# Performance work log

Hardware: AMD Instinct MI355X
Metric: run time of the kernel (lower is better)

Reference implementation:

```python
import jax, jax.numpy as jnp
import numpy as np

B, N, D = 8, 500, 256
H, W = 480, 640
NUM_CORNERS = 500
MATCH_RADIUS = 1.0
SCORE_RADIUS = 8
BETA = (1.0, 1.0, 1.0)


def _rodrigues(aa):
    theta = jnp.linalg.norm(aa, axis=-1, keepdims=True)
    k = aa / jnp.maximum(theta, 1e-8)
    kx, ky, kz = k[..., 0], k[..., 1], k[..., 2]
    z = jnp.zeros_like(kx)
    Km = jnp.stack([jnp.stack([z, -kz, ky], -1),
                    jnp.stack([kz, z, -kx], -1),
                    jnp.stack([-ky, kx, z], -1)], -2)
    th = theta[..., None]
    return jnp.eye(3) + jnp.sin(th) * Km + (1. - jnp.cos(th)) * (Km @ Km)


def setup_inputs() -> dict:
    key = jax.random.key(0)
    ks = jax.random.split(key, 8)
    descriptors = jax.random.normal(ks[0], (B, N, D), jnp.float32)
    points = jax.random.uniform(ks[1], (B, N, 2), jnp.float32, -1.0, 1.0)
    pointness = jax.random.uniform(ks[2], (B, 1, H, W), jnp.float32) * 0.98 + 0.01
    depths_dense = jax.random.uniform(ks[3], (B, 1, H, W), jnp.float32) * 4.0 + 1.0
    imgs = jax.random.uniform(ks[4], (B, 3, H, W), jnp.float32)
    aa = jax.random.normal(ks[5], (B, 3), jnp.float32) * 0.02
    t = jax.random.normal(ks[6], (B, 3), jnp.float32) * 0.05
    R = _rodrigues(aa)
    poses = jnp.tile(jnp.eye(4, dtype=jnp.float32), (B, 1, 1))
    poses = poses.at[:, :3, :3].set(R).at[:, :3, 3].set(t)
    Kmat = jnp.tile(jnp.array([[300., 0., W / 2.], [0., 300., H / 2.], [0., 0., 1.]], jnp.float32), (B, 1, 1))
    return {"descriptors": descriptors, "points": points, "pointness": pointness,
            "depths_dense": depths_dense, "poses": poses, "K": Kmat, "imgs": imgs}


def denormalize(pts, h, w):
    return jnp.stack([(pts[..., 0] + 1.) * 0.5 * (w - 1), (pts[..., 1] + 1.) * 0.5 * (h - 1)], -1)


def normalize_pix(pts, h, w):
    return jnp.stack([2. * pts[..., 0] / (w - 1) - 1., 2. * pts[..., 1] / (h - 1) - 1.], -1)


def bilinear_sample(img, px):  # img (H,W), px (...,2) pixel coords
    x = jnp.clip(px[..., 0], 0., W - 1.)
    y = jnp.clip(px[..., 1], 0., H - 1.)
    x0 = jnp.floor(x); y0 = jnp.floor(y)
    x1 = jnp.minimum(x0 + 1., W - 1.); y1 = jnp.minimum(y0 + 1., H - 1.)
    wx = x - x0; wy = y - y0
    x0i = x0.astype(jnp.int32); x1i = x1.astype(jnp.int32)
    y0i = y0.astype(jnp.int32); y1i = y1.astype(jnp.int32)
    v00 = img[y0i, x0i]; v01 = img[y0i, x1i]
    v10 = img[y1i, x0i]; v11 = img[y1i, x1i]
    return v00 * (1 - wx) * (1 - wy) + v01 * wx * (1 - wy) + v10 * (1 - wx) * wy + v11 * wx * wy


def pairwise_project(pts, depths, poses, Kmat):
    # pts (B,N,2) normalized; proj[i,j] = points of frame i projected into frame j
    px = denormalize(pts, H, W)
    d = jax.vmap(bilinear_sample)(depths[:, 0], px)  # (B,Np)
    Kinv = jnp.linalg.inv(Kmat)
    homog = jnp.concatenate([px, jnp.ones_like(px[..., :1])], -1)
    Xc = d[..., None] * jnp.einsum('bij,bnj->bni', Kinv, homog)
    Rm = poses[:, :3, :3]; t = poses[:, :3, 3]
    Xw = jnp.einsum('bij,bnj->bni', Rm, Xc) + t[:, None, :]
    diff = Xw[:, None, :, :] - t[None, :, None, :]           # (src,dst,Np,3)
    Xj = jnp.einsum('jba,ijnb->ijna', Rm, diff)              # R_j^T (Xw - t_j)
    uvw = jnp.einsum('jab,ijnb->ijna', Kmat, Xj)
    z = uvw[..., 2]
    zs = jnp.where(jnp.abs(z) < 1e-6, 1e-6, z)
    pn = normalize_pix(jnp.stack([uvw[..., 0] / zs, uvw[..., 1] / zs], -1), H, W)
    invis = (z <= 1e-6) | (jnp.abs(pn[..., 0]) > 1.) | (jnp.abs(pn[..., 1]) > 1.) | (d[:, None, :] <= 0.)
    return pn, invis


def conv2d_same(x, k):
    return jax.lax.conv_general_dilated(x, k[None, None].astype(x.dtype), (1, 1), 'SAME')


_SOBEL_X = np.array([[-1, 0, 1], [-2, 0, 2], [-1, 0, 1]], np.float32) / 8.


def _gauss_kernel(size=7, sigma=1.0):
    r = np.arange(size) - size // 2
    g = np.exp(-r ** 2 / (2 * sigma ** 2)); g /= g.sum()
    return np.outer(g, g).astype(np.float32)


_GAUSS = _gauss_kernel()


def gftt_response(gray):  # min-eigenvalue (Shi-Tomasi) corner response
    gx = conv2d_same(gray, jnp.asarray(_SOBEL_X))
    gy = conv2d_same(gray, jnp.asarray(_SOBEL_X.T))
    g = jnp.asarray(_GAUSS)
    dx2 = conv2d_same(gx * gx, g)
    dy2 = conv2d_same(gy * gy, g)
    dxy = conv2d_same(gx * gy, g)
    tr = dx2 + dy2
    det = dx2 * dy2 - dxy * dxy
    return 0.5 * (tr - jnp.sqrt(jnp.clip(tr * tr - 4. * det, 0.)))


def nms2d(x, k=5):
    mp = jax.lax.reduce_window(x, -jnp.inf, jax.lax.max, (1, 1, k, k), (1, 1, 1, 1), 'SAME')
    return x * (x == mp).astype(x.dtype)


def get_corners(imgs, depths, poses, Kmat):
    gray = (0.299 * imgs[:, 0] + 0.587 * imgs[:, 1] + 0.114 * imgs[:, 2])[:, None]
    c = nms2d(gftt_response(gray))
    r = SCORE_RADIUS
    blocks = c.reshape(B, 1, H // r, r, W // r, r)  # unfold/fold with stride==kernel
    bm = blocks.max(axis=(3, 5), keepdims=True)
    blocks = blocks * ((blocks > 0) & (blocks == bm)).astype(c.dtype)
    c = blocks.reshape(B, 1, H, W)
    vals, idx = jax.lax.top_k(c.reshape(B, -1), NUM_CORNERS)
    xs = (idx % W).astype(jnp.float32)
    ys = (idx // W).astype(jnp.float32)
    coords = normalize_pix(jnp.stack([xs, ys], -1), H, W)
    proj, invis = pairwise_project(coords, depths, poses, Kmat)
    proj = jnp.where(invis[..., None], -2.0, proj)
    combined = jnp.transpose(proj, (1, 0, 2, 3)).reshape(B, B * NUM_CORNERS, 2)  # per dst frame
    pix = jnp.round(denormalize(combined, H, W)).astype(jnp.int32)
    wq, hq = pix[..., 0], pix[..., 1]
    valid = wq >= 0
    v = jnp.tile(vals.reshape(-1), B).reshape(B, B * NUM_CORNERS)
    v = jnp.where(valid, v, 0.)
    hc = jnp.clip(hq, 0, H - 1)
    wc = jnp.clip(wq, 0, W - 1)
    bidx = jnp.broadcast_to(jnp.arange(B)[:, None], (B, B * NUM_CORNERS))
    target = jnp.zeros((B, H, W), imgs.dtype).at[bidx, hc, wc].max(v)
    target = nms2d(target[:, None])
    return (target > 0).astype(imgs.dtype)


def distinction_loss(desc):
    dn = desc / jnp.clip(jnp.linalg.norm(desc, axis=-1, keepdims=True), 1e-8)
    c = jnp.einsum('bnd,bmd->bnm', dn, dn)
    return jax.nn.relu(c).mean()


def match_loss(desc, points, proj, invis):
    p_src = denormalize(jax.lax.stop_gradient(points), H, W)  # (B,N,2)
    p_dst = denormalize(jax.lax.stop_gradient(proj), H, W)    # (src a, dst b, N, 2)
    diff = p_src[None, :, :, None, :] - p_dst[:, :, None, :, :]  # (a,b,n,m,2)
    m = (diff ** 2).sum(-1) <= MATCH_RADIUS ** 2
    m = m & (~invis)[:, :, :, None]                 # zero invisible rows
    n_idx = jnp.arange(N)
    m = m & (n_idx[:, None] < n_idx[None, :])       # triu(diagonal=1)
    dn = desc / jnp.clip(jnp.linalg.norm(desc, axis=-1, keepdims=True), 1e-8)
    cos = jnp.einsum('bnd,amd->abnm', dn, dn)       # cosine(desc[b,n], desc[a,m])
    mf = m.astype(desc.dtype)
    cnt = jnp.maximum(mf.sum(), 1.)
    return ((1. - cos) * mf).sum() / cnt


def bce(p, t):
    logp = jnp.maximum(jnp.log(p), -100.)
    log1p = jnp.maximum(jnp.log(1. - p), -100.)
    return -(t * logp + (1. - t) * log1p).mean()


def reference(descriptors, points, pointness, depths_dense, poses, K, imgs):
    distinction = distinction_loss(descriptors)
    target = get_corners(imgs, depths_dense, poses, K)
    cornerness = bce(pointness, target)
    proj, invis = pairwise_project(points, depths_dense, poses, K)
    match = match_loss(descriptors, points, proj, invis)
    return BETA[0] * distinction + BETA[1] * cornerness + BETA[2] * match
```

## Files before the change

kernel.cpp:

```cpp
#include <hip/hip_runtime.h>
#include <math.h>

#define BB 8
#define NN 500
#define DDIM 256
#define HH 480
#define WW 640
#define HWSZ (HH*WW)
#define BHW (BB*HWSZ)
#define NBLK 4800
#define NOVF 3392
#define NLIST (BB*NN*BB)
#define NBCE2 512
#define NCORR 125
#define NDM 66

#define PD_DIST  0
#define PD_MS    512
#define PD_MC    1024
#define PD_BCE   1536
#define PD_CORR  2560
#define PD_TOTAL 2688

typedef __attribute__((ext_vector_type(8))) short short8;
typedef __attribute__((ext_vector_type(4))) float f32x4;


static __device__ __forceinline__ float wredmaxf(float v) {
  #pragma unroll
  for (int o = 1; o < 64; o <<= 1) v = fmaxf(v, __shfl_xor(v, o, 64));
  return v;
}

static __device__ __forceinline__ double blockRedSum256(double v) {
  __shared__ double sp[4];
  __syncthreads();
  #pragma unroll
  for (int o = 32; o > 0; o >>= 1) v += __shfl_down(v, o, 64);
  int lane = threadIdx.x & 63, wid = threadIdx.x >> 6;
  if (lane == 0) sp[wid] = v;
  __syncthreads();
  double r = 0.0;
  if (threadIdx.x == 0) r = sp[0] + sp[1] + sp[2] + sp[3];
  return r;
}

static __device__ __forceinline__ unsigned short f2bf(float f) {
  unsigned u = __float_as_uint(f);
  return (unsigned short)((u + 0x7FFFu + ((u >> 16) & 1u)) >> 16);
}

static __device__ __forceinline__ float bilin(const float* __restrict__ img, float px, float py) {
  float x = fminf(fmaxf(px, 0.0f), 639.0f);
// ... 61 lines not shown
                                               float* __restrict__ psrc, float* __restrict__ pdst,
                                               int* __restrict__ minv,
                                               const float* __restrict__ pn, double* __restrict__ pd) {
  __shared__ float smem[6536];
  __shared__ float Gw[7];
  int bid = blockIdx.x, tid = threadIdx.x;
  if (bid < 2400) {
    float* sgxy = smem;
    float* gray = smem + 2888;
    float* hxx  = smem + 2888;
    float* hyy  = hxx + 1216;
    float* hxy  = hyy + 1216;
    int b = bid / 300, r = bid % 300;
    int byi = r / 20, bxi = r % 20;
    int bx = bxi*32, by = byi*32;
    if (bid < 20) {
      int g = bid*256 + tid;
      if (g == 0) *done = 0;
      for (int e = g; e < BB*64; e += 20*256) ovf[e] = 0;
      for (int e = g; e < NLIST; e += 20*256) list[e] = -1;
      for (int e = g; e < 12288; e += 20*256) {
        int bi = e / 1536, rr2 = e % 1536;
        dnb_u[(bi*512 + 500)*128 + rr2] = 0u;
      }
    }
    if (tid < 7) {
      double g[7]; double s = 0.0;
      for (int q = 0; q < 7; q++) { double rr2 = (double)(q-3); g[q] = exp(-(rr2*rr2)/2.0); s += g[q]; }
      Gw[tid] = (float)(g[tid]/s);
    }
    const float* ib = imgs + (size_t)b*3*HWSZ;
    for (int e = tid; e < 40*40; e += 256) {
      int ly = e/40, lx = e%40;
      int X = bx - 4 + lx, Y = by - 4 + ly;
      float v = 0.f;
      if (X>=0 && X<WW && Y>=0 && Y<HH) {
        int p = Y*WW + X;
        v = 0.299f*ib[p] + 0.587f*ib[HWSZ+p] + 0.114f*ib[2*HWSZ+p];
      }
      gray[ly*41+lx] = v;
    }
    __syncthreads();
    const float kxw[3][3] = {{-0.125f,0.f,0.125f},{-0.25f,0.f,0.25f},{-0.125f,0.f,0.125f}};
    for (int e = tid; e < 38*38; e += 256) {
      int rr2 = e/38, c = e%38;
      int X = bx - 3 + c, Y = by - 3 + rr2;
      float sx = 0.f, sy = 0.f;
      #pragma unroll
      for (int i = 0; i < 3; i++)
        #pragma unroll
        for (int j = 0; j < 3; j++) {
          float v = gray[(rr2+i)*41 + (c+j)];
          sx += kxw[i][j]*v;
          sy += kxw[j][i]*v;
        }
      bool in = (X>=0 && X<WW && Y>=0 && Y<HH);
      sgxy[e*2]   = in ? sx : 0.f;
      sgxy[e*2+1] = in ? sy : 0.f;
    }
    __syncthreads();
    for (int e = tid; e < 38*32; e += 256) {
      int rr2 = e >> 5, co = e & 31;
      int base = (rr2*38 + co)*2;
      float axx = 0.f, ayy = 0.f, axy = 0.f;
      #pragma unroll
      for (int j = 0; j < 7; j++) {
        float a = sgxy[base + j*2];
        float c = sgxy[base + j*2 + 1];
        float Gj = Gw[j];
        axx += Gj*(a*a); ayy += Gj*(c*c); axy += Gj*(a*c);
      }
      hxx[e] = axx; hyy[e] = ayy; hxy[e] = axy;
    }
    __syncthreads();
    int tx = tid & 31, ty = tid >> 5;
    int r0 = ty*4;
    float axx[4] = {0,0,0,0}, ayy[4] = {0,0,0,0}, axy[4] = {0,0,0,0};
    #pragma unroll
    for (int rr2 = 0; rr2 < 10; rr2++) {
      int rr3 = r0 + rr2;
      float vxx = hxx[rr3*32+tx], vyy = hyy[rr3*32+tx], vxy = hxy[rr3*32+tx];
      #pragma unroll
      for (int o = 0; o < 4; o++) {
        int i = rr2 - o;
        if (i >= 0 && i <= 6) {
          float Gi = Gw[i];
          axx[o] += Gi*vxx; ayy[o] += Gi*vyy; axy[o] += Gi*vxy;
        }
      }
    }
    #pragma unroll
    for (int o = 0; o < 4; o++) {
      float tr = axx[o] + ayy[o];
      float det = axx[o]*ayy[o] - axy[o]*axy[o];
      float disc = fmaxf(tr*tr - 4.0f*det, 0.f);
      int y = by + r0 + o;
      resp[(size_t)b*HWSZ + y*WW + (bx+tx)] = 0.5f*(tr - sqrtf(disc));
    }
  } else if (bid < 6400) {
    int row = bid - 2400;
    float v = desc[(size_t)row*DDIM + tid];
    float* sp2 = smem;
    float s = v*v;
    #pragma unroll
    for (int o = 32; o > 0; o >>= 1) s += __shfl_down(s, o, 64);
    int lane = tid & 63, wid = tid >> 6;
    if (lane == 0) sp2[wid] = s;
    __syncthreads();
    if (tid == 0) sp2[4] = fmaxf(sqrtf(sp2[0]+sp2[1]+sp2[2]+sp2[3]), 1e-8f);
    __syncthreads();
    float o = v / sp2[4];
    dn[(size_t)row*DDIM + tid] = o;
    int pr = (row/500)*512 + (row%500);
    dnb[(size_t)pr*DDIM + tid] = f2bf(o);
  } else if (bid < 6416) {
    int t = (bid - 6400)*256 + tid;
    if (t < BB*NN) {
      int a = t / NN, m = t % NN;
      float p0 = points[t*2], p1 = points[t*2+1];
      float px = (p0 + 1.0f)*0.5f*639.0f;
      float py = (p1 + 1.0f)*0.5f*479.0f;
      float Xw[3], d;
      src_compute(px, py, depths + (size_t)a*HWSZ, poses, Km, a, Xw, &d);
      psrc[t*2] = px; psrc[t*2+1] = py;
      for (int b = 0; b < BB; b++) {
        float nx, ny; bool inv;
        project_to(poses, Km, b, Xw, d, &nx, &ny, &inv);
        int o = (a*BB + b)*NN + m;
        pdst[o*2]   = (nx + 1.0f)*0.5f*639.0f;
        pdst[o*2+1] = (ny + 1.0f)*0.5f*479.0f;
        minv[o] = inv ? 1 : 0;
      }
    }
  } else {
    int blk = bid - 6416;
    int g = blk*256 + tid;
    double l = 0.0;
    for (int q = g; q < BHW/4; q += NBCE2*256) {
      float4 v = ((const float4*)pn)[q];
      l -= (double)fmaxf(logf(1.f - v.x), -100.f);
      l -= (double)fmaxf(logf(1.f - v.y), -100.f);
      l -= (double)fmaxf(logf(1.f - v.z), -100.f);
      l -= (double)fmaxf(logf(1.f - v.w), -100.f);
    }
    double s = blockRedSum256(l);
    if (tid == 0) pd[PD_BCE + blk] = s;
  }
}

__global__ __launch_bounds__(256) void k_mid(const float* __restrict__ resp, float* __restrict__ cv,
                                             int* __restrict__ ci, float* __restrict__ cvo,
                                             int* __restrict__ cio, int* __restrict__ ovf,
                                             float* __restrict__ target,
                                             const float* __restrict__ psrc, const float* __restrict__ pdst,
                                             const int* __restrict__ minv, const float* __restrict__ dn,
                                             const short* __restrict__ dnb, double* __restrict__ pd) {
  __shared__ float sbuf[3508];
  int bid = blockIdx.x, tid = threadIdx.x;
  if (bid < NDM) {
    int w = tid >> 6, lane = tid & 63;
    int gw = bid*4 + w;
    int r16 = lane & 15, koff = (lane >> 4)*8;
    double dsum = 0.0;
    for (int j = 0; j < 16; j++) {
      int jb = gw*16 + j;
      int b = jb / 528, t = jb % 528;
      int I = (int)((sqrtf(8.f*(float)t + 1.f) - 1.f)*0.5f);
      while ((I+1)*(I+2)/2 <= t) I++;
      while (I*(I+1)/2 > t) I--;
      int J = t - I*(I+1)/2;
      const short* bp = dnb + (size_t)b*512*DDIM;
      const short* ap = bp + (I*16 + r16)*DDIM + koff;
      const short* cp = bp + (J*16 + r16)*DDIM + koff;
      f32x4 acc = {0.f, 0.f, 0.f, 0.f};
      #pragma unroll
      for (int kk = 0; kk < 8; kk++) {
        short8 af = *(const short8*)(ap + kk*32);
        short8 bf = *(const short8*)(cp + kk*32);
        acc = __builtin_amdgcn_mfma_f32_16x16x32_bf16(af, bf, acc, 0, 0, 0);
      }
      float ls = fmaxf(acc[0],0.f) + fmaxf(acc[1],0.f) + fmaxf(acc[2],0.f) + fmaxf(acc[3],0.f);
      dsum += (double)ls * ((I == J) ? 1.0 : 2.0);
    }
    double s = blockRedSum256(dsum);
    if (tid == 0) pd[PD_DIST + bid] = s;
  } else if (bid < NDM + 512) {
    int mbid = bid - NDM;
    float* spd = sbuf;
    float* ssrc = sbuf + 1000;
    int* sinv = (int*)(sbuf + 2000);
    int ab = mbid & 63; int b = ab % BB; int a = ab / BB;
    int ys = mbid >> 6;
    for (int e = tid; e < NN; e += 256) {
      spd[e*2]   = pdst[(ab*NN+e)*2];
      spd[e*2+1] = pdst[(ab*NN+e)*2+1];
      sinv[e]    = minv[ab*NN+e];
      ssrc[e*2]   = psrc[(b*NN+e)*2];
      ssrc[e*2+1] = psrc[(b*NN+e)*2+1];
    }
    __syncthreads();
    double lsum = 0.0, lcnt = 0.0;
    for (int mm = ys; mm < NN; mm += 8) {
      float px = spd[mm*2], py = spd[mm*2+1];
      for (int nn = tid; nn < mm; nn += 256) {
        if (sinv[nn]) continue;
        float dx = ssrc[nn*2]   - px;
        float dy = ssrc[nn*2+1] - py;
        if (dx*dx + dy*dy <= 1.0f) {
          const float* da = dn + ((size_t)a*NN + mm)*DDIM;
          const float* db = dn + ((size_t)b*NN + nn)*DDIM;
          float dot = 0.f;
          for (int q = 0; q < DDIM; q++) dot += db[q]*da[q];
          lsum += (double)(1.0f - dot);
          lcnt += 1.0;
        }
      }
    }
    double s = blockRedSum256(lsum);
    if (tid == 0) pd[PD_MS + mbid] = s;
    double c2 = blockRedSum256(lcnt);
    if (tid == 0) pd[PD_MC + mbid] = c2;
  } else {
    int nb = bid - (NDM + 512);
    int b = nb / 300, r = nb % 300;
    int byi = r / 20, bxi = r % 20;
    int bx = bxi*32, by = byi*32;
    float* s = sbuf;
    float* hm = sbuf + 1332;
    float* c32 = sbuf + 2484;
    const float* rp = resp + (size_t)b*HWSZ;
    for (int e = tid; e < 36*36; e += 256) {
      int ly = e/36, lx = e%36;
      int X = bx - 2 + lx, Y = by - 2 + ly;
      s[ly*37+lx] = (X>=0 && X<WW && Y>=0 && Y<HH) ? rp[Y*WW+X] : -INFINITY;
    }
    __syncthreads();
    for (int e = tid; e < 36*32; e += 256) {
      int rr = e >> 5, co = e & 31;
      int base = rr*37 + co;
      float m = s[base];
      m = fmaxf(m, s[base+1]); m = fmaxf(m, s[base+2]);
      m = fmaxf(m, s[base+3]); m = fmaxf(m, s[base+4]);
      hm[e] = m;
    }
    __syncthreads();
    for (int e = tid; e < 1024; e += 256) {
      int y = e >> 5, x = e & 31;
      float mp = hm[y*32+x];
      mp = fmaxf(mp, hm[(y+1)*32+x]); mp = fmaxf(mp, hm[(y+2)*32+x]);
      mp = fmaxf(mp, hm[(y+3)*32+x]); mp = fmaxf(mp, hm[(y+4)*32+x]);
      float v = s[(y+2)*37 + (x+2)];
      c32[e] = (v == mp) ? v : 0.f;
      target[(size_t)b*HWSZ + (by+y)*WW + (bx+x)] = 0.f;
    }
    __syncthreads();
    int wv = tid >> 6, lane = tid & 63;
    int ly8 = lane >> 3, lx8 = lane & 7;
    for (int q = 0; q < 4; q++) {
      int bb = wv*4 + q;
      int oy = (bb >> 2)*8, ox = (bb & 3)*8;
      float cval = c32[(oy+ly8)*32 + ox+lx8];
      float bm = wredmaxf(cval);
      bool win = (cval > 0.f) && (cval == bm);
      unsigned long long mask = __ballot(win);
      int BY = byi*4 + (bb >> 2), BX = bxi*4 + (bb & 3);
      int rblk = BY*80 + BX;
      int gidx = (by+oy+ly8)*WW + (bx+ox+lx8);
      if (mask == 0ull) {
        if (lane == 0) { cv[b*NBLK+rblk] = 0.f; ci[b*NBLK+rblk] = 0; }
      } else if (win) {
        int rank = __popcll(mask & ((1ull << lane) - 1ull));
        if (rank == 0) { cv[b*NBLK+rblk] = cval; ci[b*NBLK+rblk] = gidx; }
        else {
          int pos = atomicAdd(&ovf[b*64], 1);
          if (pos < NOVF) { cvo[b*NOVF+pos] = cval; cio[b*NOVF+pos] = gidx; }
        }
      }
    }
  }
}

__global__ __launch_bounds__(1024) void k_topscat(const float* __restrict__ cv, const int* __restrict__ ci,
                                                  const float* __restrict__ cvo, const int* __restrict__ cio,
                                                  const int* __restrict__ ovf,
                                                  const float* __restrict__ depths, const float* __restrict__ poses,
                                                  const float* __restrict__ Km,
                                                  unsigned int* __restrict__ target, int* __restrict__ list) {
  __shared__ unsigned int hist[16*257];
  __shared__ unsigned int histsum[256];
  __shared__ unsigned long long prefix_s;
  __shared__ int kk_s, fin_s, cgt_s, ceq_s;
  __shared__ float s_topv[NN];
  __shared__ int s_topi[NN];
  int b = blockIdx.x;
  int tid = threadIdx.x;
  int w257 = (tid >> 6)*257;
  int nval = min(ovf[b*64], NOVF);
  unsigned long long kreg[8];
  #pragma unroll
  for (int q = 0; q < 8; q++) {
    int e = tid + q*1024;
    float v = 0.f; unsigned int idx = 0u;
    if (e < NBLK) { v = cv[b*NBLK+e]; idx = (unsigned int)ci[b*NBLK+e]; }
    else if (e - NBLK < nval) { v = cvo[b*NOVF+e-NBLK]; idx = (unsigned int)cio[b*NOVF+e-NBLK]; }
    kreg[q] = ((unsigned long long)__float_as_uint(v) << 32) | (0xFFFFFFFFu - idx);
  }
  if (tid == 0) { prefix_s = 0ull; kk_s = NN; fin_s = -1; cgt_s = 0; ceq_s = 0; }
  for (int e = tid; e < 16*257; e += 1024) hist[e] = 0u;
  __syncthreads();
  for (int round = 0; round < 8; round++) {
    int shift = 56 - 8*round;
    unsigned long long prefix = prefix_s;
    int kk = kk_s;
    unsigned long long himask = (round == 0) ? 0ull : (~0ull << (shift + 8));
    #pragma unroll
    for (int q = 0; q < 8; q++)
      if ((kreg[q] & himask) == prefix)
        atomicAdd(&hist[w257 + (unsigned int)((kreg[q] >> shift) & 255ull)], 1u);
    __syncthreads();
    if (tid < 256) {
      unsigned s = 0u;
      #pragma unroll
      for (int ww = 0; ww < 16; ww++) s += hist[ww*257 + tid];
      histsum[tid] = s;
    }
    __syncthreads();
    for (int e = tid; e < 16*257; e += 1024) hist[e] = 0u;
    if (tid < 64) {
      int l = tid;
      unsigned s0 = histsum[l], s1 = histsum[64+l], s2 = histsum[128+l], s3 = histsum[192+l];
      #pragma unroll
      for (int off = 1; off < 64; off <<= 1) {
        unsigned t0 = __shfl_down(s0, off, 64), t1 = __shfl_down(s1, off, 64);
        unsigned t2 = __shfl_down(s2, off, 64), t3 = __shfl_down(s3, off, 64);
        if (l + off < 64) { s0 += t0; s1 += t1; s2 += t2; s3 += t3; }
      }
      unsigned S1 = __shfl(s1, 0, 64), S2 = __shfl(s2, 0, 64), S3 = __shfl(s3, 0, 64);
      unsigned suf0 = s0 + S1 + S2 + S3, suf1 = s1 + S2 + S3, suf2 = s2 + S3, suf3 = s3;
      int best = -1;
      if      (suf3 >= (unsigned)kk) best = 192 + l;
      else if (suf2 >= (unsigned)kk) best = 128 + l;
      else if (suf1 >= (unsigned)kk) best = 64 + l;
      else if (suf0 >= (unsigned)kk) best = l;
      #pragma unroll
      for (int off = 1; off < 64; off <<= 1) best = max(best, __shfl_xor(best, off, 64));
      if (l == (best & 63)) {
        int seg = best >> 6;
        unsigned sufb = (seg == 3) ? suf3 : ((seg == 2) ? suf2 : ((seg == 1) ? suf1 : suf0));
        unsigned c = histsum[best];
        int Sn = (int)(sufb - c);
        int kkn = kk - Sn;
        prefix_s = prefix | ((unsigned long long)best << shift);
        kk_s = kkn;
        if (kkn == (int)c) fin_s = shift;
      }
    }
    __syncthreads();
    if (fin_s >= 0) break;
  }
  int sg = (fin_s > 0) ? fin_s : 0;
  unsigned long long prefix = prefix_s;
  int kk = kk_s;
  unsigned long long low = (sg > 0) ? ((1ull << sg) - 1ull) : 0ull;
  unsigned long long Tfull = prefix | low;
  unsigned long long mhi = ~low;
  int lane = tid & 63;
  unsigned long long lmask = (1ull << lane) - 1ull;
  #pragma unroll
  for (int q = 0; q < 8; q++) {
    unsigned long long key = kreg[q];
    bool gt = key > Tfull;
    bool eq = !gt && ((key & mhi) == prefix);
    unsigned long long mg = __ballot(gt);
    unsigned long long me = __ballot(eq);
    int slot = -1;
    if (mg != 0ull) {
      int ldr = __ffsll((long long)mg) - 1;
      int baseg = 0;
      if (lane == ldr) baseg = atomicAdd(&cgt_s, (int)__popcll(mg));
      baseg = __shfl(baseg, ldr, 64);
      if (gt) slot = baseg + (int)__popcll(mg & lmask);
    }
    if (me != 0ull) {
      int ldr = __ffsll((long long)me) - 1;
      int basee = 0;
      if (lane == ldr) basee = atomicAdd(&ceq_s, (int)__popcll(me));
      basee = __shfl(basee, ldr, 64);
      if (eq) {
        int p = basee + (int)__popcll(me & lmask);
        if (p < kk) slot = (NN-1) - p;
      }
    }
    if (slot >= 0) {
      s_topv[slot] = __uint_as_float((unsigned int)(key >> 32));
      s_topi[slot] = (int)(0xFFFFFFFFu - (unsigned int)(key & 0xFFFFFFFFull));
    }
  }
  __syncthreads();
  if (tid < NN) {
    float val = s_topv[tid];
    if (val > 0.f) {
      int idx = s_topi[tid];
      float xs = (float)(idx % WW), ys = (float)(idx / WW);
      float cx = 2.0f*xs/639.0f - 1.0f;
      float cy = 2.0f*ys/479.0f - 1.0f;
      float px = (cx + 1.0f)*0.5f*639.0f;
      float py = (cy + 1.0f)*0.5f*479.0f;
      float Xw[3], d;
      src_compute(px, py, depths + (size_t)b*HWSZ, poses, Km, b, Xw, &d);
      int tglob = b*NN + tid;
      for (int j = 0; j < BB; j++) {
        float nx, ny; bool inv;
        project_to(poses, Km, j, Xw, d, &nx, &ny, &inv);
        if (inv) { nx = -2.0f; ny = -2.0f; }
        float fx = rintf((nx + 1.0f)*0.5f*639.0f);
        float fy = rintf((ny + 1.0f)*0.5f*479.0f);
        int wq = (int)fx, hq = (int)fy;
        if (wq < 0) continue;
        int hc = min(max(hq, 0), HH-1), wc = min(max(wq, 0), WW-1);
        int p = j*HWSZ + hc*WW + wc;
        unsigned int old = atomicMax(&target[p], __float_as_uint(val));
        if (old == 0u) list[tglob*BB + j] = p;
      }
    }
  }
}

__global__ __launch_bounds__(256) void k_last(const int* __restrict__ list, const float* __restrict__ target,
                                              const float* __restrict__ pn, double* __restrict__ pd,
                                              int* __restrict__ done, float* __restrict__ out) {
  __shared__ int lastf;
  int blk = blockIdx.x, tid = threadIdx.x;
  int g = blk*256 + tid;
  double l = 0.0;
  if (g < NLIST) {
    int p = list[g];
    if (p >= 0) {
      int j = p / HWSZ, pix = p % HWSZ;
// ... 13 lines not shown
        l = (double)(-fmaxf(logf(pv), -100.f)) + (double)fmaxf(logf(1.f - pv), -100.f);
      }
    }
  }
  double s = blockRedSum256(l);
  if (tid == 0) {
    pd[PD_CORR + blk] = s;
    __threadfence();
    int t = atomicAdd(done, 1);
    lastf = (t == NCORR - 1) ? 1 : 0;
  }
  __syncthreads();
  if (lastf) {
    __threadfence();
    double l2;
    l2 = 0.0; for (int i = tid; i < NDM;   i += 256) l2 += pd[PD_DIST + i];
    double dist = blockRedSum256(l2);
    l2 = 0.0; for (int i = tid; i < 512;   i += 256) l2 += pd[PD_MS + i];
    double ms = blockRedSum256(l2);
    l2 = 0.0; for (int i = tid; i < 512;   i += 256) l2 += pd[PD_MC + i];
    double mc = blockRedSum256(l2);
    l2 = 0.0; for (int i = tid; i < NBCE2; i += 256) l2 += pd[PD_BCE + i];
    double bce = blockRedSum256(l2);
    l2 = 0.0; for (int i = tid; i < NCORR; i += 256) l2 += pd[PD_CORR + i];
    double corr = blockRedSum256(l2);
    if (tid == 0) {
      float distf = (float)(dist / (double)(BB*NN*NN));
      float cornf = (float)((bce + corr) / (double)BHW);
      float cntf  = fmaxf((float)mc, 1.0f);
      float matchf = (float)ms / cntf;
      out[0] = distf + cornf + matchf;
// ... 20 lines not shown
  float* bufA = f;
  float* bufC = bufA + (size_t)BHW;
  float* cv_main = bufC + (size_t)BHW;
  int*   ci_main = (int*)(cv_main + BB*NBLK);
  float* cv_ovf  = (float*)(ci_main + BB*NBLK);
  int*   ci_ovf  = (int*)(cv_ovf + BB*NOVF);
  int*   ovf     = (int*)(ci_ovf + BB*NOVF);
  float* psrc = (float*)(ovf + BB*64);
  float* pdst = psrc + BB*NN*2;
  int*   minv = (int*)(pdst + BB*BB*NN*2);
  float* dn   = (float*)(minv + BB*BB*NN);
  int*   list = (int*)(dn + (size_t)BB*NN*DDIM);
  unsigned short* dnb = (unsigned short*)(list + NLIST);
  int*   done = (int*)(dnb + (size_t)BB*512*DDIM);

  k_front  <<<6928, 256, 0, stream>>>(imgs, bufA, ovf, list, (unsigned int*)dnb, done,
                                      desc, dn, dnb, points, depths, poses, Kmat,
                                      psrc, pdst, minv, pointness, pd);
  k_mid    <<<NDM + 512 + 2400, 256, 0, stream>>>(bufA, cv_main, ci_main, cv_ovf, ci_ovf, ovf, bufC,
                                                  psrc, pdst, minv, dn, (const short*)dnb, pd);
  k_topscat<<<BB, 1024, 0, stream>>>(cv_main, ci_main, cv_ovf, ci_ovf, ovf,
                                     depths, poses, Kmat, (unsigned int*)bufC, list);
  k_last   <<<NCORR, 256, 0, stream>>>(list, bufC, pointness, pd, done, out);
}
```

Measured before the change: 110.5 us.

## Split NMS from distinction/match work and co-schedule them with top-k selection

The mid stage is split. NMS now runs in its own 2400-block kernel, and the distinction MFMA and match-loss blocks move into a 1024-thread kernel that also runs the per-batch top-k radix select and scatter. The long serial top-k blocks can therefore overlap with the descriptor work instead of running alone. The descriptor normalization now handles four rows per block with float4 loads, and the Harris front stage uses 2D row/column thread indexing. Together these add work to a big-block kernel, and the changed block granularity may shift occupancy.

```diff
diff --git a/kernel.cpp b/kernel.cpp
--- a/kernel.cpp
+++ b/kernel.cpp
@@ -13,7 +13,8 @@
 #define NLIST (BB*NN*BB)
 #define NBCE2 512
 #define NCORR 125
-#define NDM 66
+#define ND17 17
+#define NDJOBW 264
 
 #define PD_DIST  0
 #define PD_MS    512
@@ -32,11 +33,16 @@
   return v;
 }
 
+static __device__ __forceinline__ double wredsumd(double v) {
+  #pragma unroll
+  for (int o = 32; o > 0; o >>= 1) v += __shfl_down(v, o, 64);
+  return v;
+}
+
 static __device__ __forceinline__ double blockRedSum256(double v) {
   __shared__ double sp[4];
   __syncthreads();
-  #pragma unroll
-  for (int o = 32; o > 0; o >>= 1) v += __shfl_down(v, o, 64);
+  v = wredsumd(v);
   int lane = threadIdx.x & 63, wid = threadIdx.x >> 6;
   if (lane == 0) sp[wid] = v;
   __syncthreads();
@@ -128,6 +134,7 @@
     int b = bid / 300, r = bid % 300;
     int byi = r / 20, bxi = r % 20;
     int bx = bxi*32, by = byi*32;
+    int tx = tid & 31, ty = tid >> 5;
     if (bid < 20) {
       int g = bid*256 + tid;
       if (g == 0) *done = 0;
@@ -144,38 +151,44 @@
       Gw[tid] = (float)(g[tid]/s);
     }
     const float* ib = imgs + (size_t)b*3*HWSZ;
-    for (int e = tid; e < 40*40; e += 256) {
-      int ly = e/40, lx = e%40;
-      int X = bx - 4 + lx, Y = by - 4 + ly;
-      float v = 0.f;
-      if (X>=0 && X<WW && Y>=0 && Y<HH) {
-        int p = Y*WW + X;
-        v = 0.299f*ib[p] + 0.587f*ib[HWSZ+p] + 0.114f*ib[2*HWSZ+p];
-      }
-      gray[ly*41+lx] = v;
+    for (int ly = ty; ly < 40; ly += 8) {
+      int Y = by - 4 + ly;
+      bool yin = (Y >= 0 && Y < HH);
+      for (int lx = tx; lx < 40; lx += 32) {
+        int X = bx - 4 + lx;
+        float v = 0.f;
+        if (yin && X >= 0 && X < WW) {
+          int p = Y*WW + X;
+          v = 0.299f*ib[p] + 0.587f*ib[HWSZ+p] + 0.114f*ib[2*HWSZ+p];
+        }
+        gray[ly*41+lx] = v;
+      }
     }
     __syncthreads();
     const float kxw[3][3] = {{-0.125f,0.f,0.125f},{-0.25f,0.f,0.25f},{-0.125f,0.f,0.125f}};
-    for (int e = tid; e < 38*38; e += 256) {
-      int rr2 = e/38, c = e%38;
-      int X = bx - 3 + c, Y = by - 3 + rr2;
-      float sx = 0.f, sy = 0.f;
-      #pragma unroll
-      for (int i = 0; i < 3; i++)
+    for (int ly = ty; ly < 38; ly += 8) {
+      int Y = by - 3 + ly;
+      bool yin = (Y >= 0 && Y < HH);
+      for (int lx = tx; lx < 38; lx += 32) {
+        int X = bx - 3 + lx;
+        float sx = 0.f, sy = 0.f;
         #pragma unroll
-        for (int j = 0; j < 3; j++) {
-          float v = gray[(rr2+i)*41 + (c+j)];
-          sx += kxw[i][j]*v;
-          sy += kxw[j][i]*v;
-        }
-      bool in = (X>=0 && X<WW && Y>=0 && Y<HH);
-      sgxy[e*2]   = in ? sx : 0.f;
-      sgxy[e*2+1] = in ? sy : 0.f;
-    }
-    __syncthreads();
-    for (int e = tid; e < 38*32; e += 256) {
-      int rr2 = e >> 5, co = e & 31;
-      int base = (rr2*38 + co)*2;
+        for (int i = 0; i < 3; i++)
+          #pragma unroll
+          for (int j = 0; j < 3; j++) {
+            float v = gray[(ly+i)*41 + (lx+j)];
+            sx += kxw[i][j]*v;
+            sy += kxw[j][i]*v;
+          }
+        bool in = yin && (X >= 0 && X < WW);
+        int e = ly*38 + lx;
+        sgxy[e*2]   = in ? sx : 0.f;
+        sgxy[e*2+1] = in ? sy : 0.f;
+      }
+    }
+    __syncthreads();
+    for (int rr2 = ty; rr2 < 38; rr2 += 8) {
+      int base = (rr2*38 + tx)*2;
       float axx = 0.f, ayy = 0.f, axy = 0.f;
       #pragma unroll
       for (int j = 0; j < 7; j++) {
@@ -184,10 +197,10 @@
         float Gj = Gw[j];
         axx += Gj*(a*a); ayy += Gj*(c*c); axy += Gj*(a*c);
       }
+      int e = rr2*32 + tx;
       hxx[e] = axx; hyy[e] = ayy; hxy[e] = axy;
     }
     __syncthreads();
-    int tx = tid & 31, ty = tid >> 5;
     int r0 = ty*4;
     float axx[4] = {0,0,0,0}, ayy[4] = {0,0,0,0}, axy[4] = {0,0,0,0};
     #pragma unroll
@@ -211,24 +224,23 @@
       int y = by + r0 + o;
       resp[(size_t)b*HWSZ + y*WW + (bx+tx)] = 0.5f*(tr - sqrtf(disc));
     }
-  } else if (bid < 6400) {
-    int row = bid - 2400;
-    float v = desc[(size_t)row*DDIM + tid];
-    float* sp2 = smem;
-    float s = v*v;
+  } else if (bid < 3400) {
+    int row = (bid - 2400)*4 + (tid >> 6);
+    int lane = tid & 63;
+    float4 v4 = *(const float4*)&desc[(size_t)row*DDIM + lane*4];
+    float s = v4.x*v4.x + v4.y*v4.y + v4.z*v4.z + v4.w*v4.w;
     #pragma unroll
     for (int o = 32; o > 0; o >>= 1) s += __shfl_down(s, o, 64);
-    int lane = tid & 63, wid = tid >> 6;
-    if (lane == 0) sp2[wid] = s;
-    __syncthreads();
-    if (tid == 0) sp2[4] = fmaxf(sqrtf(sp2[0]+sp2[1]+sp2[2]+sp2[3]), 1e-8f);
-    __syncthreads();
-    float o = v / sp2[4];
-    dn[(size_t)row*DDIM + tid] = o;
+    s = __shfl(s, 0, 64);
+    float den = fmaxf(sqrtf(s), 1e-8f);
+    float4 o4 = make_float4(v4.x/den, v4.y/den, v4.z/den, v4.w/den);
+    *(float4*)&dn[(size_t)row*DDIM + lane*4] = o4;
     int pr = (row/500)*512 + (row%500);
-    dnb[(size_t)pr*DDIM + tid] = f2bf(o);
-  } else if (bid < 6416) {
-    int t = (bid - 6400)*256 + tid;
+    unsigned lo = (unsigned)f2bf(o4.x) | ((unsigned)f2bf(o4.y) << 16);
+    unsigned hi = (unsigned)f2bf(o4.z) | ((unsigned)f2bf(o4.w) << 16);
+    *(uint2*)&dnb[(size_t)pr*DDIM + lane*4] = make_uint2(lo, hi);
+  } else if (bid < 3416) {
+    int t = (bid - 3400)*256 + tid;
     if (t < BB*NN) {
       int a = t / NN, m = t % NN;
       float p0 = points[t*2], p1 = points[t*2+1];
@@ -247,7 +259,7 @@
       }
     }
   } else {
-    int blk = bid - 6416;
+    int blk = bid - 3416;
     int g = blk*256 + tid;
     double l = 0.0;
     for (int q = g; q < BHW/4; q += NBCE2*256) {
@@ -262,50 +274,265 @@
   }
 }
 
-__global__ __launch_bounds__(256) void k_mid(const float* __restrict__ resp, float* __restrict__ cv,
+__global__ __launch_bounds__(256) void k_nms(const float* __restrict__ resp, float* __restrict__ cv,
                                              int* __restrict__ ci, float* __restrict__ cvo,
                                              int* __restrict__ cio, int* __restrict__ ovf,
-                                             float* __restrict__ target,
-                                             const float* __restrict__ psrc, const float* __restrict__ pdst,
-                                             const int* __restrict__ minv, const float* __restrict__ dn,
-                                             const short* __restrict__ dnb, double* __restrict__ pd) {
+                                             float* __restrict__ target) {
   __shared__ float sbuf[3508];
   int bid = blockIdx.x, tid = threadIdx.x;
-  if (bid < NDM) {
-    int w = tid >> 6, lane = tid & 63;
-    int gw = bid*4 + w;
+  int b = bid / 300, r = bid % 300;
+  int byi = r / 20, bxi = r % 20;
+  int bx = bxi*32, by = byi*32;
+  float* s = sbuf;
+  float* hm = sbuf + 1332;
+  float* c32 = sbuf + 2484;
+  const float* rp = resp + (size_t)b*HWSZ;
+  for (int e = tid; e < 36*36; e += 256) {
+    int ly = e/36, lx = e%36;
+    int X = bx - 2 + lx, Y = by - 2 + ly;
+    s[ly*37+lx] = (X>=0 && X<WW && Y>=0 && Y<HH) ? rp[Y*WW+X] : -INFINITY;
+  }
+  __syncthreads();
+  for (int e = tid; e < 36*32; e += 256) {
+    int rr = e >> 5, co = e & 31;
+    int base = rr*37 + co;
+    float m = s[base];
+    m = fmaxf(m, s[base+1]); m = fmaxf(m, s[base+2]);
+    m = fmaxf(m, s[base+3]); m = fmaxf(m, s[base+4]);
+    hm[e] = m;
+  }
+  __syncthreads();
+  for (int e = tid; e < 1024; e += 256) {
+    int y = e >> 5, x = e & 31;
+    float mp = hm[y*32+x];
+    mp = fmaxf(mp, hm[(y+1)*32+x]); mp = fmaxf(mp, hm[(y+2)*32+x]);
+    mp = fmaxf(mp, hm[(y+3)*32+x]); mp = fmaxf(mp, hm[(y+4)*32+x]);
+    float v = s[(y+2)*37 + (x+2)];
+    c32[e] = (v == mp) ? v : 0.f;
+    target[(size_t)b*HWSZ + (by+y)*WW + (bx+x)] = 0.f;
+  }
+  __syncthreads();
+  int wv = tid >> 6, lane = tid & 63;
+  int ly8 = lane >> 3, lx8 = lane & 7;
+  for (int q = 0; q < 4; q++) {
+    int bb = wv*4 + q;
+    int oy = (bb >> 2)*8, ox = (bb & 3)*8;
+    float cval = c32[(oy+ly8)*32 + ox+lx8];
+    float bm = wredmaxf(cval);
+    bool win = (cval > 0.f) && (cval == bm);
+    unsigned long long mask = __ballot(win);
+    int BY = byi*4 + (bb >> 2), BX = bxi*4 + (bb & 3);
+    int rblk = BY*80 + BX;
+    int gidx = (by+oy+ly8)*WW + (bx+ox+lx8);
+    if (mask == 0ull) {
+      if (lane == 0) { cv[b*NBLK+rblk] = 0.f; ci[b*NBLK+rblk] = 0; }
+    } else if (win) {
+      int rank = __popcll(mask & ((1ull << lane) - 1ull));
+      if (rank == 0) { cv[b*NBLK+rblk] = cval; ci[b*NBLK+rblk] = gidx; }
+      else {
+        int pos = atomicAdd(&ovf[b*64], 1);
+        if (pos < NOVF) { cvo[b*NOVF+pos] = cval; cio[b*NOVF+pos] = gidx; }
+      }
+    }
+  }
+}
+
+__global__ __launch_bounds__(1024) void k_combo(const float* __restrict__ cv, const int* __restrict__ ci,
+                                                const float* __restrict__ cvo, const int* __restrict__ cio,
+                                                const int* __restrict__ ovf,
+                                                const float* __restrict__ depths, const float* __restrict__ poses,
+                                                const float* __restrict__ Km,
+                                                unsigned int* __restrict__ target, int* __restrict__ list,
+                                                const float* __restrict__ psrc, const float* __restrict__ pdst,
+                                                const int* __restrict__ minv, const float* __restrict__ dn,
+                                                const short* __restrict__ dnb, double* __restrict__ pd) {
+  __shared__ double sraw[5056];
+  __shared__ unsigned long long prefix_s;
+  __shared__ int kk_s, fin_s, cgt_s, ceq_s;
+  int bid = blockIdx.x, tid = threadIdx.x;
+  if (bid < 8) {
+    unsigned int* hist = (unsigned int*)sraw;
+    unsigned int* histsum = hist + 16*257;
+    float* s_topv = (float*)(histsum + 256);
+    int* s_topi = (int*)(s_topv + NN);
+    int b = bid;
+    int w257 = (tid >> 6)*257;
+    int nval = min(ovf[b*64], NOVF);
+    unsigned long long kreg[8];
+    #pragma unroll
+    for (int q = 0; q < 8; q++) {
+      int e = tid + q*1024;
+      float v = 0.f; unsigned int idx = 0u;
+      if (e < NBLK) { v = cv[b*NBLK+e]; idx = (unsigned int)ci[b*NBLK+e]; }
+      else if (e - NBLK < nval) { v = cvo[b*NOVF+e-NBLK]; idx = (unsigned int)cio[b*NOVF+e-NBLK]; }
+      kreg[q] = ((unsigned long long)__float_as_uint(v) << 32) | (0xFFFFFFFFu - idx);
+    }
+    if (tid == 0) { prefix_s = 0ull; kk_s = NN; fin_s = -1; cgt_s = 0; ceq_s = 0; }
+    for (int e = tid; e < 16*257; e += 1024) hist[e] = 0u;
+    __syncthreads();
+    for (int round = 0; round < 8; round++) {
+      int shift = 56 - 8*round;
+      unsigned long long prefix = prefix_s;
+      int kk = kk_s;
+      unsigned long long himask = (round == 0) ? 0ull : (~0ull << (shift + 8));
+      #pragma unroll
+      for (int q = 0; q < 8; q++)
+        if ((kreg[q] & himask) == prefix)
+          atomicAdd(&hist[w257 + (unsigned int)((kreg[q] >> shift) & 255ull)], 1u);
+      __syncthreads();
+      if (tid < 256) {
+        unsigned s = 0u;
+        #pragma unroll
+        for (int ww = 0; ww < 16; ww++) s += hist[ww*257 + tid];
+        histsum[tid] = s;
+      }
+      __syncthreads();
+      for (int e = tid; e < 16*257; e += 1024) hist[e] = 0u;
+      if (tid < 64) {
+        int l = tid;
+        unsigned s0 = histsum[l], s1 = histsum[64+l], s2 = histsum[128+l], s3 = histsum[192+l];
+        #pragma unroll
+        for (int off = 1; off < 64; off <<= 1) {
+          unsigned t0 = __shfl_down(s0, off, 64), t1 = __shfl_down(s1, off, 64);
+          unsigned t2 = __shfl_down(s2, off, 64), t3 = __shfl_down(s3, off, 64);
+          if (l + off < 64) { s0 += t0; s1 += t1; s2 += t2; s3 += t3; }
+        }
+        unsigned S1 = __shfl(s1, 0, 64), S2 = __shfl(s2, 0, 64), S3 = __shfl(s3, 0, 64);
+        unsigned suf0 = s0 + S1 + S2 + S3, suf1 = s1 + S2 + S3, suf2 = s2 + S3, suf3 = s3;
+        int best = -1;
+        if      (suf3 >= (unsigned)kk) best = 192 + l;
+        else if (suf2 >= (unsigned)kk) best = 128 + l;
+        else if (suf1 >= (unsigned)kk) best = 64 + l;
+        else if (suf0 >= (unsigned)kk) best = l;
+        #pragma unroll
+        for (int off = 1; off < 64; off <<= 1) best = max(best, __shfl_xor(best, off, 64));
+        if (l == (best & 63)) {
+          int seg = best >> 6;
+          unsigned sufb = (seg == 3) ? suf3 : ((seg == 2) ? suf2 : ((seg == 1) ? suf1 : suf0));
+          unsigned c = histsum[best];
+          int Sn = (int)(sufb - c);
+          int kkn = kk - Sn;
+          prefix_s = prefix | ((unsigned long long)best << shift);
+          kk_s = kkn;
+          if (kkn == (int)c) fin_s = shift;
+        }
+      }
+      __syncthreads();
+      if (fin_s >= 0) break;
+    }
+    int sg = (fin_s > 0) ? fin_s : 0;
+    unsigned long long prefix = prefix_s;
+    int kk = kk_s;
+    unsigned long long low = (sg > 0) ? ((1ull << sg) - 1ull) : 0ull;
+    unsigned long long Tfull = prefix | low;
+    unsigned long long mhi = ~low;
+    int lane = tid & 63;
+    unsigned long long lmask = (1ull << lane) - 1ull;
+    #pragma unroll
+    for (int q = 0; q < 8; q++) {
+      unsigned long long key = kreg[q];
+      bool gt = key > Tfull;
+      bool eq = !gt && ((key & mhi) == prefix);
+      unsigned long long mg = __ballot(gt);
+      unsigned long long me = __ballot(eq);
+      int slot = -1;
+      if (mg != 0ull) {
+        int ldr = __ffsll((long long)mg) - 1;
+        int baseg = 0;
+        if (lane == ldr) baseg = atomicAdd(&cgt_s, (int)__popcll(mg));
+        baseg = __shfl(baseg, ldr, 64);
+        if (gt) slot = baseg + (int)__popcll(mg & lmask);
+      }
+      if (me != 0ull) {
+        int ldr = __ffsll((long long)me) - 1;
+        int basee = 0;
+        if (lane == ldr) basee = atomicAdd(&ceq_s, (int)__popcll(me));
+        basee = __shfl(basee, ldr, 64);
+        if (eq) {
+          int p = basee + (int)__popcll(me & lmask);
+          if (p < kk) slot = (NN-1) - p;
+        }
+      }
+      if (slot >= 0) {
+        s_topv[slot] = __uint_as_float((unsigned int)(key >> 32));
+        s_topi[slot] = (int)(0xFFFFFFFFu - (unsigned int)(key & 0xFFFFFFFFull));
+      }
+    }
+    __syncthreads();
+    if (tid < NN) {
+      float val = s_topv[tid];
+      if (val > 0.f) {
+        int idx = s_topi[tid];
+        float xs = (float)(idx % WW), ys = (float)(idx / WW);
+        float cx = 2.0f*xs/639.0f - 1.0f;
+        float cy = 2.0f*ys/479.0f - 1.0f;
+        float px = (cx + 1.0f)*0.5f*639.0f;
+        float py = (cy + 1.0f)*0.5f*479.0f;
+        float Xw[3], d;
+        src_compute(px, py, depths + (size_t)b*HWSZ, poses, Km, b, Xw, &d);
+        int tglob = b*NN + tid;
+        for (int j = 0; j < BB; j++) {
+          float nx, ny; bool inv;
+          project_to(poses, Km, j, Xw, d, &nx, &ny, &inv);
+          if (inv) { nx = -2.0f; ny = -2.0f; }
+          float fx = rintf((nx + 1.0f)*0.5f*639.0f);
+          float fy = rintf((ny + 1.0f)*0.5f*479.0f);
+          int wq = (int)fx, hq = (int)fy;
+          if (wq < 0) continue;
+          int hc = min(max(hq, 0), HH-1), wc = min(max(wq, 0), WW-1);
+          int p = j*HWSZ + hc*WW + wc;
+          unsigned int old = atomicMax(&target[p], __float_as_uint(val));
+          if (old == 0u) list[tglob*BB + j] = p;
+        }
+      }
+    }
+  } else if (bid < 8 + ND17) {
+    int w16 = tid >> 6, lane = tid & 63;
+    int gw = (bid - 8)*16 + w16;
     int r16 = lane & 15, koff = (lane >> 4)*8;
     double dsum = 0.0;
-    for (int j = 0; j < 16; j++) {
-      int jb = gw*16 + j;
-      int b = jb / 528, t = jb % 528;
-      int I = (int)((sqrtf(8.f*(float)t + 1.f) - 1.f)*0.5f);
-      while ((I+1)*(I+2)/2 <= t) I++;
-      while (I*(I+1)/2 > t) I--;
-      int J = t - I*(I+1)/2;
-      const short* bp = dnb + (size_t)b*512*DDIM;
-      const short* ap = bp + (I*16 + r16)*DDIM + koff;
-      const short* cp = bp + (J*16 + r16)*DDIM + koff;
-      f32x4 acc = {0.f, 0.f, 0.f, 0.f};
+    if (gw < NDJOBW) {
+      for (int j = 0; j < 16; j++) {
+        int jb = gw*16 + j;
+        int b = jb / 528, t = jb % 528;
+        int I = (int)((sqrtf(8.f*(float)t + 1.f) - 1.f)*0.5f);
+        while ((I+1)*(I+2)/2 <= t) I++;
+        while (I*(I+1)/2 > t) I--;
+        int J = t - I*(I+1)/2;
+        const short* bp = dnb + (size_t)b*512*DDIM;
+        const short* ap = bp + (I*16 + r16)*DDIM + koff;
+        const short* cp = bp + (J*16 + r16)*DDIM + koff;
+        f32x4 acc = {0.f, 0.f, 0.f, 0.f};
+        #pragma unroll
+        for (int kk = 0; kk < 8; kk++) {
+          short8 af = *(const short8*)(ap + kk*32);
+          short8 bf = *(const short8*)(cp + kk*32);
+          acc = __builtin_amdgcn_mfma_f32_16x16x32_bf16(af, bf, acc, 0, 0, 0);
+        }
+        float ls = fmaxf(acc[0],0.f) + fmaxf(acc[1],0.f) + fmaxf(acc[2],0.f) + fmaxf(acc[3],0.f);
+        dsum += (double)ls * ((I == J) ? 1.0 : 2.0);
+      }
+    }
+    dsum = wredsumd(dsum);
+    double* dsp = sraw;
+    if (lane == 0) dsp[w16] = dsum;
+    __syncthreads();
+    if (tid == 0) {
+      double s = 0.0;
       #pragma unroll
-      for (int kk = 0; kk < 8; kk++) {
-        short8 af = *(const short8*)(ap + kk*32);
-        short8 bf = *(const short8*)(cp + kk*32);
-        acc = __builtin_amdgcn_mfma_f32_16x16x32_bf16(af, bf, acc, 0, 0, 0);
-      }
-      float ls = fmaxf(acc[0],0.f) + fmaxf(acc[1],0.f) + fmaxf(acc[2],0.f) + fmaxf(acc[3],0.f);
-      dsum += (double)ls * ((I == J) ? 1.0 : 2.0);
-    }
-    double s = blockRedSum256(dsum);
-    if (tid == 0) pd[PD_DIST + bid] = s;
-  } else if (bid < NDM + 512) {
-    int mbid = bid - NDM;
-    float* spd = sbuf;
-    float* ssrc = sbuf + 1000;
-    int* sinv = (int*)(sbuf + 2000);
+      for (int i = 0; i < 16; i++) s += dsp[i];
+      pd[PD_DIST + (bid - 8)] = s;
+    }
+  } else {
+    int sub = tid >> 8, st = tid & 255;
+    int mbid = (bid - (8 + ND17))*4 + sub;
+    float* bb = (float*)sraw + sub*2500;
+    float* spd = bb;
+    float* ssrc = bb + 1000;
+    int* sinv = (int*)(bb + 2000);
     int ab = mbid & 63; int b = ab % BB; int a = ab / BB;
     int ys = mbid >> 6;
-    for (int e = tid; e < NN; e += 256) {
+    for (int e = st; e < NN; e += 256) {
       spd[e*2]   = pdst[(ab*NN+e)*2];
       spd[e*2+1] = pdst[(ab*NN+e)*2+1];
       sinv[e]    = minv[ab*NN+e];
@@ -316,7 +543,7 @@
     double lsum = 0.0, lcnt = 0.0;
     for (int mm = ys; mm < NN; mm += 8) {
       float px = spd[mm*2], py = spd[mm*2+1];
-      for (int nn = tid; nn < mm; nn += 256) {
+      for (int nn = st; nn < mm; nn += 256) {
         if (sinv[nn]) continue;
         float dx = ssrc[nn*2]   - px;
         float dy = ssrc[nn*2+1] - py;
@@ -330,212 +557,18 @@
         }
       }
     }
-    double s = blockRedSum256(lsum);
-    if (tid == 0) pd[PD_MS + mbid] = s;
-    double c2 = blockRedSum256(lcnt);
-    if (tid == 0) pd[PD_MC + mbid] = c2;
-  } else {
-    int nb = bid - (NDM + 512);
-    int b = nb / 300, r = nb % 300;
-    int byi = r / 20, bxi = r % 20;
-    int bx = bxi*32, by = byi*32;
-    float* s = sbuf;
-    float* hm = sbuf + 1332;
-    float* c32 = sbuf + 2484;
-    const float* rp = resp + (size_t)b*HWSZ;
-    for (int e = tid; e < 36*36; e += 256) {
-      int ly = e/36, lx = e%36;
-      int X = bx - 2 + lx, Y = by - 2 + ly;
-      s[ly*37+lx] = (X>=0 && X<WW && Y>=0 && Y<HH) ? rp[Y*WW+X] : -INFINITY;
-    }
-    __syncthreads();
-    for (int e = tid; e < 36*32; e += 256) {
-      int rr = e >> 5, co = e & 31;
-      int base = rr*37 + co;
-      float m = s[base];
-      m = fmaxf(m, s[base+1]); m = fmaxf(m, s[base+2]);
-      m = fmaxf(m, s[base+3]); m = fmaxf(m, s[base+4]);
-      hm[e] = m;
-    }
-    __syncthreads();
-    for (int e = tid; e < 1024; e += 256) {
-      int y = e >> 5, x = e & 31;
-      float mp = hm[y*32+x];
-      mp = fmaxf(mp, hm[(y+1)*32+x]); mp = fmaxf(mp, hm[(y+2)*32+x]);
-      mp = fmaxf(mp, hm[(y+3)*32+x]); mp = fmaxf(mp, hm[(y+4)*32+x]);
-      float v = s[(y+2)*37 + (x+2)];
-      c32[e] = (v == mp) ? v : 0.f;
-      target[(size_t)b*HWSZ + (by+y)*WW + (bx+x)] = 0.f;
-    }
-    __syncthreads();
-    int wv = tid >> 6, lane = tid & 63;
-    int ly8 = lane >> 3, lx8 = lane & 7;
-    for (int q = 0; q < 4; q++) {
-      int bb = wv*4 + q;
-      int oy = (bb >> 2)*8, ox = (bb & 3)*8;
-      float cval = c32[(oy+ly8)*32 + ox+lx8];
-      float bm = wredmaxf(cval);
-      bool win = (cval > 0.f) && (cval == bm);
-      unsigned long long mask = __ballot(win);
-      int BY = byi*4 + (bb >> 2), BX = bxi*4 + (bb & 3);
-      int rblk = BY*80 + BX;
-      int gidx = (by+oy+ly8)*WW + (bx+ox+lx8);
-      if (mask == 0ull) {
-        if (lane == 0) { cv[b*NBLK+rblk] = 0.f; ci[b*NBLK+rblk] = 0; }
-      } else if (win) {
-        int rank = __popcll(mask & ((1ull << lane) - 1ull));
-        if (rank == 0) { cv[b*NBLK+rblk] = cval; ci[b*NBLK+rblk] = gidx; }
-        else {
-          int pos = atomicAdd(&ovf[b*64], 1);
-          if (pos < NOVF) { cvo[b*NOVF+pos] = cval; cio[b*NOVF+pos] = gidx; }
-        }
-      }
-    }
-  }
-}
-
-__global__ __launch_bounds__(1024) void k_topscat(const float* __restrict__ cv, const int* __restrict__ ci,
-                                                  const float* __restrict__ cvo, const int* __restrict__ cio,
-                                                  const int* __restrict__ ovf,
-                                                  const float* __restrict__ depths, const float* __restrict__ poses,
-                                                  const float* __restrict__ Km,
-                                                  unsigned int* __restrict__ target, int* __restrict__ list) {
-  __shared__ unsigned int hist[16*257];
-  __shared__ unsigned int histsum[256];
-  __shared__ unsigned long long prefix_s;
-  __shared__ int kk_s, fin_s, cgt_s, ceq_s;
-  __shared__ float s_topv[NN];
-  __shared__ int s_topi[NN];
-  int b = blockIdx.x;
-  int tid = threadIdx.x;
-  int w257 = (tid >> 6)*257;
-  int nval = min(ovf[b*64], NOVF);
-  unsigned long long kreg[8];
-  #pragma unroll
-  for (int q = 0; q < 8; q++) {
-    int e = tid + q*1024;
-    float v = 0.f; unsigned int idx = 0u;
-    if (e < NBLK) { v = cv[b*NBLK+e]; idx = (unsigned int)ci[b*NBLK+e]; }
-    else if (e - NBLK < nval) { v = cvo[b*NOVF+e-NBLK]; idx = (unsigned int)cio[b*NOVF+e-NBLK]; }
-    kreg[q] = ((unsigned long long)__float_as_uint(v) << 32) | (0xFFFFFFFFu - idx);
-  }
-  if (tid == 0) { prefix_s = 0ull; kk_s = NN; fin_s = -1; cgt_s = 0; ceq_s = 0; }
-  for (int e = tid; e < 16*257; e += 1024) hist[e] = 0u;
-  __syncthreads();
-  for (int round = 0; round < 8; round++) {
-    int shift = 56 - 8*round;
-    unsigned long long prefix = prefix_s;
-    int kk = kk_s;
-    unsigned long long himask = (round == 0) ? 0ull : (~0ull << (shift + 8));
-    #pragma unroll
-    for (int q = 0; q < 8; q++)
-      if ((kreg[q] & himask) == prefix)
-        atomicAdd(&hist[w257 + (unsigned int)((kreg[q] >> shift) & 255ull)], 1u);
-    __syncthreads();
-    if (tid < 256) {
-      unsigned s = 0u;
+    double ls = wredsumd(lsum);
+    double lc = wredsumd(lcnt);
+    double* rd = (double*)((float*)sraw + 10048);
+    int wv = tid >> 6;
+    if ((tid & 63) == 0) { rd[wv] = ls; rd[16+wv] = lc; }
+    __syncthreads();
+    if (st == 0) {
+      double s = 0.0, c = 0.0;
       #pragma unroll
-      for (int ww = 0; ww < 16; ww++) s += hist[ww*257 + tid];
-      histsum[tid] = s;
-    }
-    __syncthreads();
-    for (int e = tid; e < 16*257; e += 1024) hist[e] = 0u;
-    if (tid < 64) {
-      int l = tid;
-      unsigned s0 = histsum[l], s1 = histsum[64+l], s2 = histsum[128+l], s3 = histsum[192+l];
-      #pragma unroll
-      for (int off = 1; off < 64; off <<= 1) {
-        unsigned t0 = __shfl_down(s0, off, 64), t1 = __shfl_down(s1, off, 64);
-        unsigned t2 = __shfl_down(s2, off, 64), t3 = __shfl_down(s3, off, 64);
-        if (l + off < 64) { s0 += t0; s1 += t1; s2 += t2; s3 += t3; }
-      }
-      unsigned S1 = __shfl(s1, 0, 64), S2 = __shfl(s2, 0, 64), S3 = __shfl(s3, 0, 64);
-      unsigned suf0 = s0 + S1 + S2 + S3, suf1 = s1 + S2 + S3, suf2 = s2 + S3, suf3 = s3;
-      int best = -1;
-      if      (suf3 >= (unsigned)kk) best = 192 + l;
-      else if (suf2 >= (unsigned)kk) best = 128 + l;
-      else if (suf1 >= (unsigned)kk) best = 64 + l;
-      else if (suf0 >= (unsigned)kk) best = l;
-      #pragma unroll
-      for (int off = 1; off < 64; off <<= 1) best = max(best, __shfl_xor(best, off, 64));
-      if (l == (best & 63)) {
-        int seg = best >> 6;
-        unsigned sufb = (seg == 3) ? suf3 : ((seg == 2) ? suf2 : ((seg == 1) ? suf1 : suf0));
-        unsigned c = histsum[best];
-        int Sn = (int)(sufb - c);
-        int kkn = kk - Sn;
-        prefix_s = prefix | ((unsigned long long)best << shift);
-        kk_s = kkn;
-        if (kkn == (int)c) fin_s = shift;
-      }
-    }
-    __syncthreads();
-    if (fin_s >= 0) break;
-  }
-  int sg = (fin_s > 0) ? fin_s : 0;
-  unsigned long long prefix = prefix_s;
-  int kk = kk_s;
-  unsigned long long low = (sg > 0) ? ((1ull << sg) - 1ull) : 0ull;
-  unsigned long long Tfull = prefix | low;
-  unsigned long long mhi = ~low;
-  int lane = tid & 63;
-  unsigned long long lmask = (1ull << lane) - 1ull;
-  #pragma unroll
-  for (int q = 0; q < 8; q++) {
-    unsigned long long key = kreg[q];
-    bool gt = key > Tfull;
-    bool eq = !gt && ((key & mhi) == prefix);
-    unsigned long long mg = __ballot(gt);
-    unsigned long long me = __ballot(eq);
-    int slot = -1;
-    if (mg != 0ull) {
-      int ldr = __ffsll((long long)mg) - 1;
-      int baseg = 0;
-      if (lane == ldr) baseg = atomicAdd(&cgt_s, (int)__popcll(mg));
-      baseg = __shfl(baseg, ldr, 64);
-      if (gt) slot = baseg + (int)__popcll(mg & lmask);
-    }
-    if (me != 0ull) {
-      int ldr = __ffsll((long long)me) - 1;
-      int basee = 0;
-      if (lane == ldr) basee = atomicAdd(&ceq_s, (int)__popcll(me));
-      basee = __shfl(basee, ldr, 64);
-      if (eq) {
-        int p = basee + (int)__popcll(me & lmask);
-        if (p < kk) slot = (NN-1) - p;
-      }
-    }
-    if (slot >= 0) {
-      s_topv[slot] = __uint_as_float((unsigned int)(key >> 32));
-      s_topi[slot] = (int)(0xFFFFFFFFu - (unsigned int)(key & 0xFFFFFFFFull));
-    }
-  }
-  __syncthreads();
-  if (tid < NN) {
-    float val = s_topv[tid];
-    if (val > 0.f) {
-      int idx = s_topi[tid];
-      float xs = (float)(idx % WW), ys = (float)(idx / WW);
-      float cx = 2.0f*xs/639.0f - 1.0f;
-      float cy = 2.0f*ys/479.0f - 1.0f;
-      float px = (cx + 1.0f)*0.5f*639.0f;
-      float py = (cy + 1.0f)*0.5f*479.0f;
-      float Xw[3], d;
-      src_compute(px, py, depths + (size_t)b*HWSZ, poses, Km, b, Xw, &d);
-      int tglob = b*NN + tid;
-      for (int j = 0; j < BB; j++) {
-        float nx, ny; bool inv;
-        project_to(poses, Km, j, Xw, d, &nx, &ny, &inv);
-        if (inv) { nx = -2.0f; ny = -2.0f; }
-        float fx = rintf((nx + 1.0f)*0.5f*639.0f);
-        float fy = rintf((ny + 1.0f)*0.5f*479.0f);
-        int wq = (int)fx, hq = (int)fy;
-        if (wq < 0) continue;
-        int hc = min(max(hq, 0), HH-1), wc = min(max(wq, 0), WW-1);
-        int p = j*HWSZ + hc*WW + wc;
-        unsigned int old = atomicMax(&target[p], __float_as_uint(val));
-        if (old == 0u) list[tglob*BB + j] = p;
-      }
+      for (int i = 0; i < 4; i++) { s += rd[sub*4+i]; c += rd[16+sub*4+i]; }
+      pd[PD_MS + mbid] = s;
+      pd[PD_MC + mbid] = c;
     }
   }
 }
@@ -579,7 +612,7 @@
   if (lastf) {
     __threadfence();
     double l2;
-    l2 = 0.0; for (int i = tid; i < NDM;   i += 256) l2 += pd[PD_DIST + i];
+    l2 = 0.0; for (int i = tid; i < ND17;  i += 256) l2 += pd[PD_DIST + i];
     double dist = blockRedSum256(l2);
     l2 = 0.0; for (int i = tid; i < 512;   i += 256) l2 += pd[PD_MS + i];
     double ms = blockRedSum256(l2);
@@ -630,12 +663,12 @@
   unsigned short* dnb = (unsigned short*)(list + NLIST);
   int*   done = (int*)(dnb + (size_t)BB*512*DDIM);
 
-  k_front  <<<6928, 256, 0, stream>>>(imgs, bufA, ovf, list, (unsigned int*)dnb, done,
-                                      desc, dn, dnb, points, depths, poses, Kmat,
-                                      psrc, pdst, minv, pointness, pd);
-  k_mid    <<<NDM + 512 + 2400, 256, 0, stream>>>(bufA, cv_main, ci_main, cv_ovf, ci_ovf, ovf, bufC,
-                                                  psrc, pdst, minv, dn, (const short*)dnb, pd);
-  k_topscat<<<BB, 1024, 0, stream>>>(cv_main, ci_main, cv_ovf, ci_ovf, ovf,
-                                     depths, poses, Kmat, (unsigned int*)bufC, list);
-  k_last   <<<NCORR, 256, 0, stream>>>(list, bufC, pointness, pd, done, out);
-}
+  k_front<<<3928, 256, 0, stream>>>(imgs, bufA, ovf, list, (unsigned int*)dnb, done,
+                                    desc, dn, dnb, points, depths, poses, Kmat,
+                                    psrc, pdst, minv, pointness, pd);
+  k_nms  <<<2400, 256, 0, stream>>>(bufA, cv_main, ci_main, cv_ovf, ci_ovf, ovf, bufC);
+  k_combo<<<8 + ND17 + 128, 1024, 0, stream>>>(cv_main, ci_main, cv_ovf, ci_ovf, ovf,
+                                               depths, poses, Kmat, (unsigned int*)bufC, list,
+                                               psrc, pdst, minv, dn, (const short*)dnb, pd);
+  k_last <<<NCORR, 256, 0, stream>>>(list, bufC, pointness, pd, done, out);
+}
```

Result: slower. 176.2 us (+59.5%).
